# Performance work log

Hardware: AMD Instinct MI355X
Metric: run time of the kernel (lower is better)

The kernel has to match this reference:

```python
import jax, jax.numpy as jnp
import numpy as np
import math

B, S, H, D = 8, 2048, 1024, 64  # batch, seq_len, hidden_dim, head_size

def setup_inputs() -> dict:
    key = jax.random.key(0)
    ks = jax.random.split(key, 7)
    lim = 1.0 / math.sqrt(H)  # torch Linear default init bound
    return {
        "x":  jax.random.normal(ks[0], (B, S, H), dtype=jnp.float32),
        "Wq": jax.random.uniform(ks[1], (H, D), jnp.float32, -lim, lim),
        "bq": jax.random.uniform(ks[2], (D,),   jnp.float32, -lim, lim),
        "Wk": jax.random.uniform(ks[3], (H, D), jnp.float32, -lim, lim),
        "bk": jax.random.uniform(ks[4], (D,),   jnp.float32, -lim, lim),
        "Wv": jax.random.uniform(ks[5], (H, D), jnp.float32, -lim, lim),
        "bv": jax.random.uniform(ks[6], (D,),   jnp.float32, -lim, lim),
    }

def reference(x, Wq, bq, Wk, bk, Wv, bv):
    # x: [B, S, H]
    q = x @ Wq + bq          # [B, S, D]
    k = x @ Wk + bk          # [B, S, D]
    v = x @ Wv + bv          # [B, S, D]
    scores = jnp.einsum("bsd,btd->bst", q, k)       # [B, S, S]
    causal = jnp.tril(jnp.ones((S, S), dtype=bool))
    scores = jnp.where(causal, scores, -jnp.inf)
    # NOTE: original module (faithfully) applies softmax FIRST, then divides
    # by sqrt(hidden_dim) -- it does NOT scale logits before softmax.
    weight = jax.nn.softmax(scores, axis=-1) / jnp.sqrt(jnp.float32(x.shape[-1]))
    # dropout p=0.0 -> identity
    return jnp.einsum("bst,btd->bsd", weight, v)     # [B, S, D]
```

## Files before the change

### kernel.cpp

```cpp
#include <hip/hip_runtime.h>


typedef float     f32x4 __attribute__((ext_vector_type(4)));
typedef _Float16  f16x8 __attribute__((ext_vector_type(8)));
typedef _Float16  f16x4 __attribute__((ext_vector_type(4)));

__global__ __launch_bounds__(256) void wt_prep(const float* __restrict__ Wq,
                                               const float* __restrict__ Wk,
                                               const float* __restrict__ Wv,
                                               _Float16* __restrict__ WtF) {
  const int w  = blockIdx.x >> 4;
  const int kt = blockIdx.x & 15;
  const float* src = (w == 0) ? Wq : (w == 1 ? Wk : Wv);
  __shared__ _Float16 ls[64][72];
  const int t = threadIdx.x;
  {
    int rr = t >> 4;
    int c4 = (t & 15) * 4;
    #pragma unroll
    for (int ri = 0; ri < 4; ++ri) {
      int k = rr + ri * 16;
      f32x4 f = *(const f32x4*)&src[(size_t)(kt * 64 + k) * 64 + c4];
      #pragma unroll
      for (int j = 0; j < 4; ++j) ls[k][c4 + j] = (_Float16)f[j];
    }
  }
  __syncthreads();
  const int lane = t & 63, l16 = lane & 15, quad = lane >> 4;
  #pragma unroll
  for (int h = 0; h < 2; ++h) {
    int fid     = h * 4 + (t >> 6);
    int kstep_l = fid >> 2;
    int ntl     = fid & 3;
    int nt      = w * 4 + ntl;
    int kstep   = kt * 2 + kstep_l;
    f16x8 o;
    #pragma unroll
    for (int j = 0; j < 8; ++j) o[j] = ls[kstep_l * 32 + quad * 8 + j][ntl * 16 + l16];
    *(f16x8*)&WtF[((size_t)(kstep * 12 + nt) * 64 + lane) * 8] = o;
  }
}

__global__ __launch_bounds__(512, 4) void qkv_gemm(const float* __restrict__ x,
                                                   const _Float16* __restrict__ WtF,
                                                   const float* __restrict__ bq,
                                                   const float* __restrict__ bk,
                                                   const float* __restrict__ bv,
                                                   _Float16* __restrict__ qo,
                                                   _Float16* __restrict__ ko,
                                                   _Float16* __restrict__ vt) {
  __shared__ _Float16 xs[32 * 1024];
  const int tid  = threadIdx.x;
  const int wave = tid >> 6, lane = tid & 63;
  const int l16  = lane & 15, quad = lane >> 4;
  const int mhalf = wave >> 2;
  const int ngrp  = wave & 3;
  const int bid   = blockIdx.x;
  const int m0    = (((bid & 7) << 6) + (bid >> 3)) * 32;

  {
    int row   = tid >> 4;
    int cbase = (tid & 15) * 4;
    const float* xrow = x + (size_t)(m0 + row) * 1024;
    int key = row & 7;
    #pragma unroll
    for (int j = 0; j < 16; ++j) {
      int col = cbase + j * 64;
      f32x4 f = *(const f32x4*)&xrow[col];
      f16x4 hh;
      #pragma unroll
      for (int e = 0; e < 4; ++e) hh[e] = (_Float16)f[e];
      int g   = col >> 3;
      int sub = col & 7;
      *(f16x4*)&xs[(size_t)row * 1024 + (size_t)((g ^ key) << 3) + sub] = hh;
    }
  }
  __syncthreads();

  f32x4 acc0 = (f32x4){0.f,0.f,0.f,0.f};
  f32x4 acc1 = (f32x4){0.f,0.f,0.f,0.f};
  f32x4 acc2 = (f32x4){0.f,0.f,0.f,0.f};

  const int arow = mhalf * 16 + l16;
  const _Float16* abase = xs + (size_t)arow * 1024;
  const int akey = arow & 7;
  const _Float16* wbase = WtF + ((size_t)(ngrp * 3) * 64 + lane) * 8;

  #pragma unroll 4
  for (int kstep = 0; kstep < 32; ++kstep) {
    f16x8 a = *(const f16x8*)(abase + (((kstep * 4 + quad) ^ akey) << 3));
    const _Float16* wk = wbase + (size_t)kstep * (12 * 64 * 8);
    f16x8 b0 = *(const f16x8*)(wk);
    f16x8 b1 = *(const f16x8*)(wk + 512);
    f16x8 b2 = *(const f16x8*)(wk + 1024);
    acc0 = __builtin_amdgcn_mfma_f32_16x16x32_f16(a, b0, acc0, 0, 0, 0);
    acc1 = __builtin_amdgcn_mfma_f32_16x16x32_f16(a, b1, acc1, 0, 0, 0);
    acc2 = __builtin_amdgcn_mfma_f32_16x16x32_f16(a, b2, acc2, 0, 0, 0);
  }

  f32x4 accs[3] = {acc0, acc1, acc2};
  #pragma unroll
  for (int i = 0; i < 3; ++i) {
    int nt  = ngrp * 3 + i;
    int col = nt * 16 + l16;
    float bias = (nt < 4) ? bq[col] : (nt < 8) ? bk[col - 64] : bv[col - 128];
    #pragma unroll
    for (int r = 0; r < 4; ++r) {
      int m = m0 + mhalf * 16 + quad * 4 + r;
      _Float16 hv = (_Float16)(accs[i][r] + bias);
      if (nt < 4)      qo[(size_t)m * 64 + col] = hv;
      else if (nt < 8) ko[(size_t)m * 64 + (col - 64)] = hv;
      else {
        int b = m >> 11, s = m & 2047;
        vt[((size_t)b * 64 + (col - 128)) * 2048 + s] = hv;
      }
    }
  }
}

__global__ __launch_bounds__(256, 2) void attn(const _Float16* __restrict__ q,
                                               const _Float16* __restrict__ k,
                                               const _Float16* __restrict__ vt,
                                               float* __restrict__ out) {
  const int blk  = blockIdx.x;
  const int pair = blk >> 3;
  const int b    = blk & 7;
  const int tid  = threadIdx.x;
  const int w    = tid >> 6, lane = tid & 63;
  const int l16  = lane & 15, quad = lane >> 4;
  const int whichq = w >> 1;
  const int half   = w & 1;
  const int qt   = whichq ? (127 - pair) : pair;
  const int q0   = qt * 16;
  const int qrow = q0 + l16;
  const int nt   = (qt >> 2) + 1;
  const int nh0  = (nt + 1) >> 1;
  const int t0   = half ? nh0 : 0;
  const int t1   = half ? nt : nh0;

  __shared__ __align__(16) unsigned char sbuf[4][4352];
  __shared__ float mlb[4][2][16];
  _Float16 (*Pw)[72]  = (_Float16 (*)[72])&sbuf[w][0];
  float    (*obw)[68] = (float    (*)[68])&sbuf[w][0];

  const _Float16* qb = q  + (size_t)b * 2048 * 64;
  const _Float16* kb = k  + (size_t)b * 2048 * 64;
  const _Float16* vb = vt + (size_t)b * 64 * 2048;

  const f16x8 qf0 = *(const f16x8*)&qb[(q0 + l16) * 64 + quad * 8];
  const f16x8 qf1 = *(const f16x8*)&qb[(q0 + l16) * 64 + 32 + quad * 8];

  const float L2E = 1.44269504088896340736f;
  float m = -1e30f, l = 0.f;
  f32x4 o_[4];
  #pragma unroll
  for (int i = 0; i < 4; ++i) o_[i] = (f32x4){0.f, 0.f, 0.f, 0.f};

  f16x8 kfA[4][2], kfB[4][2], vfA[2][4], vfB[2][4];

  auto LOADT = [&](f16x8 (&kf)[4][2], f16x8 (&vf)[2][4], int t) {
    const int kvb = t * 64;
    #pragma unroll
    for (int st = 0; st < 4; ++st) {
      kf[st][0] = *(const f16x8*)&kb[(kvb + st * 16 + l16) * 64 + quad * 8];
      kf[st][1] = *(const f16x8*)&kb[(kvb + st * 16 + l16) * 64 + 32 + quad * 8];
    }
    #pragma unroll
    for (int ks = 0; ks < 2; ++ks)
      #pragma unroll
      for (int dt = 0; dt < 4; ++dt)
        vf[ks][dt] = *(const f16x8*)&vb[(size_t)(dt * 16 + l16) * 2048 + kvb + ks * 32 + quad * 8];
  };

  auto COMPUTE = [&](const f16x8 (&kf)[4][2], const f16x8 (&vf)[2][4], int t) {
    const int kvb = t * 64;
    f32x4 sc[4];
    #pragma unroll
    for (int st = 0; st < 4; ++st) {
      f32x4 cc = (f32x4){0.f, 0.f, 0.f, 0.f};
      cc = __builtin_amdgcn_mfma_f32_16x16x32_f16(kf[st][0], qf0, cc, 0, 0, 0);
      cc = __builtin_amdgcn_mfma_f32_16x16x32_f16(kf[st][1], qf1, cc, 0, 0, 0);
      sc[st] = cc;
    }
    if (kvb + 63 > q0) {
      #pragma unroll
      for (int st = 0; st < 4; ++st)
        #pragma unroll
        for (int r = 0; r < 4; ++r)
          if (kvb + st * 16 + quad * 4 + r > qrow) sc[st][r] = -1e30f;
    }
    float mx = -1e30f;
    #pragma unroll
    for (int st = 0; st < 4; ++st)
      mx = fmaxf(mx, fmaxf(fmaxf(sc[st][0], sc[st][1]), fmaxf(sc[st][2], sc[st][3])));
    mx = fmaxf(mx, __shfl_xor(mx, 16, 64));
    mx = fmaxf(mx, __shfl_xor(mx, 32, 64));
    const float mnew  = fmaxf(m, mx);
    const float alpha = exp2f((m - mnew) * L2E);
    m = mnew;
    float s = 0.f;
    #pragma unroll
    for (int st = 0; st < 4; ++st) {
      #pragma unroll
      for (int r = 0; r < 4; ++r) sc[st][r] = exp2f((sc[st][r] - m) * L2E);
      s += (sc[st][0] + sc[st][1]) + (sc[st][2] + sc[st][3]);
    }
    s += __shfl_xor(s, 16, 64);
    s += __shfl_xor(s, 32, 64);
    l = l * alpha + s;
    #pragma unroll
    for (int dt = 0; dt < 4; ++dt)
      #pragma unroll
      for (int r = 0; r < 4; ++r) o_[dt][r] *= alpha;
    #pragma unroll
    for (int st = 0; st < 4; ++st) {
      f16x4 ph;
      #pragma unroll
      for (int r = 0; r < 4; ++r) ph[r] = (_Float16)sc[st][r];
      *(f16x4*)&Pw[l16][st * 16 + quad * 4] = ph;
    }
    asm volatile("s_waitcnt lgkmcnt(0)" ::: "memory");
    __builtin_amdgcn_sched_barrier(0);
    #pragma unroll
    for (int ks = 0; ks < 2; ++ks) {
      f16x8 pf = *(const f16x8*)&Pw[l16][ks * 32 + quad * 8];
      #pragma unroll
      for (int dt = 0; dt < 4; ++dt)
        o_[dt] = __builtin_amdgcn_mfma_f32_16x16x32_f16(vf[ks][dt], pf, o_[dt], 0, 0, 0);
    }
  };

  int t = t0;
  if (t < t1) {
    LOADT(kfA, vfA, t);
    while (t + 1 < t1) {
      LOADT(kfB, vfB, t + 1);
      __builtin_amdgcn_sched_barrier(0);
      COMPUTE(kfA, vfA, t);
      if (t + 2 < t1) {
        LOADT(kfA, vfA, t + 2);
        __builtin_amdgcn_sched_barrier(0);
      }
      COMPUTE(kfB, vfB, t + 1);
      t += 2;
    }
    if (t < t1) COMPUTE(kfA, vfA, t);
  }

  #pragma unroll
  for (int dt = 0; dt < 4; ++dt)
    *(f32x4*)&obw[l16][dt * 16 + quad * 4] = o_[dt];
  if (quad == 0) {
    mlb[w][0][l16] = m;
    mlb[w][1][l16] = l;
  }
  __syncthreads();

  {
    const int grp = tid >> 7;
    const int idx = tid & 127;
    const int row = idx >> 3;
    const int c8  = (idx & 7) * 8;
    const int wb  = grp * 2;
    const int qtg = grp ? (127 - pair) : pair;
    const float m0v = mlb[wb][0][row], m1v = mlb[wb + 1][0][row];
    const float M   = fmaxf(m0v, m1v);
    const float w0  = exp2f((m0v - M) * L2E);
    const float w1  = exp2f((m1v - M) * L2E);
    const float L   = w0 * mlb[wb][1][row] + w1 * mlb[wb + 1][1][row];
    const float inv = 1.0f / (L * 32.0f);
    const float (*oA)[68] = (const float (*)[68])&sbuf[wb][0];
    const float (*oB)[68] = (const float (*)[68])&sbuf[wb + 1][0];
    float* dst = out + ((size_t)b * 2048 + qtg * 16 + row) * 64 + c8;
    #pragma unroll
    for (int j = 0; j < 2; ++j) {
      f32x4 a = *(const f32x4*)&oA[row][c8 + j * 4];
      f32x4 bb = *(const f32x4*)&oB[row][c8 + j * 4];
      f32x4 r;
      #pragma unroll
      for (int e = 0; e < 4; ++e) r[e] = (w0 * a[e] + w1 * bb[e]) * inv;
      *(f32x4*)&dst[j * 4] = r;
    }
  }
}

extern "C" void kernel_launch(void* const* d_in, const int* in_sizes, int n_in,
                              void* d_out, int out_size, void* d_ws, size_t ws_size,
                              hipStream_t stream) {
  const float* x  = (const float*)d_in[0];
  const float* Wq = (const float*)d_in[1];
  const float* bq = (const float*)d_in[2];
  const float* Wk = (const float*)d_in[3];
  const float* bk = (const float*)d_in[4];
  const float* Wv = (const float*)d_in[5];
  const float* bv = (const float*)d_in[6];
  float* out = (float*)d_out;

  _Float16* WtF = (_Float16*)d_ws;
  _Float16* qo  = WtF + 192 * 1024;
  _Float16* ko  = qo + 16384 * 64;
  _Float16* vt  = ko + 16384 * 64;

  hipLaunchKernelGGL(wt_prep,  dim3(48),  dim3(256), 0, stream, Wq, Wk, Wv, WtF);
  hipLaunchKernelGGL(qkv_gemm, dim3(512), dim3(512), 0, stream, x, WtF, bq, bk, bv, qo, ko, vt);
  hipLaunchKernelGGL(attn,     dim3(512), dim3(256), 0, stream, qo, ko, vt, out);
}
```

Baseline: 150.8 us.

## Store Q/K/V in MFMA fragment-packed layout for contiguous attention loads

The QKV GEMM epilogue now writes Q, K and V directly into a layout pre-arranged as per-lane MFMA fragments, 512 halves per 16x32 tile. The attention kernel then loads each f16x8 operand as one contiguous 16-byte-per-lane read, replacing strided row gathers. This is meant to improve memory coalescing and simplify address arithmetic in the attention inner loop. In exchange the GEMM epilogue does scattered scalar half stores with more complex indexing.

```diff
diff --git a/kernel.cpp b/kernel.cpp
--- a/kernel.cpp
+++ b/kernel.cpp
@@ -46,9 +46,9 @@
                                                    const float* __restrict__ bq,
                                                    const float* __restrict__ bk,
                                                    const float* __restrict__ bv,
-                                                   _Float16* __restrict__ qo,
-                                                   _Float16* __restrict__ ko,
-                                                   _Float16* __restrict__ vt) {
+                                                   _Float16* __restrict__ qfr,
+                                                   _Float16* __restrict__ kfr,
+                                                   _Float16* __restrict__ vfr) {
   __shared__ _Float16 xs[32 * 1024];
   const int tid  = threadIdx.x;
   const int wave = tid >> 6, lane = tid & 63;
@@ -108,19 +108,26 @@
     for (int r = 0; r < 4; ++r) {
       int m = m0 + mhalf * 16 + quad * 4 + r;
       _Float16 hv = (_Float16)(accs[i][r] + bias);
-      if (nt < 4)      qo[(size_t)m * 64 + col] = hv;
-      else if (nt < 8) ko[(size_t)m * 64 + (col - 64)] = hv;
-      else {
+      if (nt < 4) {
+        qfr[((size_t)(m >> 4) * 2 + (col >> 5)) * 512
+            + (((col >> 3) & 3) * 16 + (m & 15)) * 8 + (col & 7)] = hv;
+      } else if (nt < 8) {
+        int ck = col - 64;
+        kfr[((size_t)(m >> 4) * 2 + (ck >> 5)) * 512
+            + (((ck >> 3) & 3) * 16 + (m & 15)) * 8 + (ck & 7)] = hv;
+      } else {
+        int cv = col - 128;
         int b = m >> 11, s = m & 2047;
-        vt[((size_t)b * 64 + (col - 128)) * 2048 + s] = hv;
+        vfr[(((size_t)b * 64 + (s >> 5)) * 4 + (cv >> 4)) * 512
+            + (((s >> 3) & 3) * 16 + (cv & 15)) * 8 + (s & 7)] = hv;
       }
     }
   }
 }
 
-__global__ __launch_bounds__(256, 2) void attn(const _Float16* __restrict__ q,
-                                               const _Float16* __restrict__ k,
-                                               const _Float16* __restrict__ vt,
+__global__ __launch_bounds__(256, 2) void attn(const _Float16* __restrict__ qfr,
+                                               const _Float16* __restrict__ kfr,
+                                               const _Float16* __restrict__ vfr,
                                                float* __restrict__ out) {
   const int blk  = blockIdx.x;
   const int pair = blk >> 3;
@@ -143,12 +150,12 @@
   _Float16 (*Pw)[72]  = (_Float16 (*)[72])&sbuf[w][0];
   float    (*obw)[68] = (float    (*)[68])&sbuf[w][0];
 
-  const _Float16* qb = q  + (size_t)b * 2048 * 64;
-  const _Float16* kb = k  + (size_t)b * 2048 * 64;
-  const _Float16* vb = vt + (size_t)b * 64 * 2048;
-
-  const f16x8 qf0 = *(const f16x8*)&qb[(q0 + l16) * 64 + quad * 8];
-  const f16x8 qf1 = *(const f16x8*)&qb[(q0 + l16) * 64 + 32 + quad * 8];
+  const _Float16* qb = qfr + ((size_t)(b * 128 + qt) * 2) * 512 + lane * 8;
+  const _Float16* kb = kfr + ((size_t)b * 128 * 2) * 512 + lane * 8;
+  const _Float16* vb = vfr + ((size_t)b * 64 * 4) * 512 + lane * 8;
+
+  const f16x8 qf0 = *(const f16x8*)(qb);
+  const f16x8 qf1 = *(const f16x8*)(qb + 512);
 
   const float L2E = 1.44269504088896340736f;
   float m = -1e30f, l = 0.f;
@@ -159,17 +166,18 @@
   f16x8 kfA[4][2], kfB[4][2], vfA[2][4], vfB[2][4];
 
   auto LOADT = [&](f16x8 (&kf)[4][2], f16x8 (&vf)[2][4], int t) {
-    const int kvb = t * 64;
+    const _Float16* kp = kb + (size_t)t * 4096;
     #pragma unroll
     for (int st = 0; st < 4; ++st) {
-      kf[st][0] = *(const f16x8*)&kb[(kvb + st * 16 + l16) * 64 + quad * 8];
-      kf[st][1] = *(const f16x8*)&kb[(kvb + st * 16 + l16) * 64 + 32 + quad * 8];
-    }
+      kf[st][0] = *(const f16x8*)(kp + st * 1024);
+      kf[st][1] = *(const f16x8*)(kp + st * 1024 + 512);
+    }
+    const _Float16* vp = vb + (size_t)t * 4096;
     #pragma unroll
     for (int ks = 0; ks < 2; ++ks)
       #pragma unroll
       for (int dt = 0; dt < 4; ++dt)
-        vf[ks][dt] = *(const f16x8*)&vb[(size_t)(dt * 16 + l16) * 2048 + kvb + ks * 32 + quad * 8];
+        vf[ks][dt] = *(const f16x8*)(vp + ks * 2048 + dt * 512);
   };
 
   auto COMPUTE = [&](const f16x8 (&kf)[4][2], const f16x8 (&vf)[2][4], int t) {
@@ -297,11 +305,11 @@
   float* out = (float*)d_out;
 
   _Float16* WtF = (_Float16*)d_ws;
-  _Float16* qo  = WtF + 192 * 1024;
-  _Float16* ko  = qo + 16384 * 64;
-  _Float16* vt  = ko + 16384 * 64;
+  _Float16* qfr = WtF + 192 * 1024;
+  _Float16* kfr = qfr + (size_t)8 * 128 * 2 * 512;
+  _Float16* vfr = kfr + (size_t)8 * 128 * 2 * 512;
 
   hipLaunchKernelGGL(wt_prep,  dim3(48),  dim3(256), 0, stream, Wq, Wk, Wv, WtF);
-  hipLaunchKernelGGL(qkv_gemm, dim3(512), dim3(512), 0, stream, x, WtF, bq, bk, bv, qo, ko, vt);
-  hipLaunchKernelGGL(attn,     dim3(512), dim3(256), 0, stream, qo, ko, vt, out);
+  hipLaunchKernelGGL(qkv_gemm, dim3(512), dim3(512), 0, stream, x, WtF, bq, bk, bv, qfr, kfr, vfr);
+  hipLaunchKernelGGL(attn,     dim3(512), dim3(256), 0, stream, qfr, kfr, vfr, out);
 }
```

Result: faster. 135.9 us (-9.9%).
